# Optimization experiments

Hardware: AMD Instinct MI355X
Metric: run time of the kernel (lower is better)

## Reference

```python
import jax, jax.numpy as jnp
import numpy as np

B, C, H, W = 64, 256, 56, 56
HEADS, DH, WS = 16, 16, 7  # C = HEADS*DH
EPS = 1e-6


def setup_inputs() -> dict:
    key = jax.random.key(0)
    k1, k2, k3 = jax.random.split(key, 3)
    return {
        "x": jax.random.normal(k1, (B, C, H, W), jnp.float32),
        "bn_gamma": jnp.ones((C,), jnp.float32),
        "bn_beta": jnp.zeros((C,), jnp.float32),
        "bn_mean": jnp.zeros((C,), jnp.float32),
        "bn_var": jnp.ones((C,), jnp.float32),
        "qk_w": jax.random.normal(k2, (2 * C, C), jnp.float32) * 0.02,
        "v_w": jax.random.normal(k3, (C, C), jnp.float32) * 0.02,
    }


def reference(x, bn_gamma, bn_beta, bn_mean, bn_var, qk_w, v_w):
    Bb, Cc, Hh, Ww = x.shape
    scale = DH ** -0.5
    # eval-mode BatchNorm2d (eps=1e-6)
    inv = bn_gamma / jnp.sqrt(bn_var + EPS)
    xn = (x - bn_mean[:, None, None]) * inv[:, None, None] + bn_beta[:, None, None]
    # window partition: einops '(h1 n1)' -> h1 (window coord) OUTER, n1 INNER
    # i.e. strided/grid windows; H divisible by WS so no padding (pad_r=pad_b=0)
    n1, n2 = Hh // WS, Ww // WS
    t = xn.reshape(Bb, Cc, WS, n1, WS, n2).transpose(0, 3, 5, 2, 4, 1)  # (B,n1,n2,ws,ws,C)
    tok = t.reshape(Bb * n1 * n2, WS * WS, Cc)  # per-window tokens
    # qk: 1x1 conv == matmul; channel layout (qk, heads, dim_head)
    qk = (tok @ qk_w.T).reshape(-1, WS * WS, 2, HEADS, DH)
    q = qk[:, :, 0].transpose(0, 2, 1, 3)  # (nb, heads, hw, dh)
    k = qk[:, :, 1].transpose(0, 2, 1, 3)
    attn = jax.nn.softmax(jnp.einsum('bhqd,bhkd->bhqk', q, k) * scale, axis=-1)
    # v: 1x1 conv + ReLU (attn_pre=False path)
    v = jax.nn.relu(tok @ v_w.T).reshape(-1, WS * WS, HEADS, DH).transpose(0, 2, 1, 3)
    o = jnp.einsum('bhqk,bhkd->bhqd', attn, v)  # (nb, heads, hw, dh)
    o = o.transpose(0, 2, 1, 3).reshape(Bb, n1, n2, WS, WS, Cc)
    # inverse window merge: target (B, C, ws_h, n1, ws_w, n2) -> (B, C, H, W)
    out = o.transpose(0, 5, 3, 1, 4, 2).reshape(Bb, Cc, Hh, Ww)
    return out
```

## Files before the change

kernel.cpp:

```cpp
#include <hip/hip_runtime.h>


typedef unsigned short u16;
typedef __attribute__((ext_vector_type(4))) float f32x4;
typedef __attribute__((ext_vector_type(8))) short short8;
typedef __attribute__((ext_vector_type(4))) short short4b;

__device__ __forceinline__ u16 f2bf(float f) {
  union { float f; unsigned int i; } v; v.f = f;
  unsigned int r = v.i + 0x7fffu + ((v.i >> 16) & 1u);
  return (u16)(r >> 16);
}

__global__ __launch_bounds__(256) void k0_wpack(
    const float* __restrict__ qkw, const float* __restrict__ vw,
    u16* __restrict__ wb)
{
  int idx = blockIdx.x * 256 + threadIdx.x;
  int n = idx >> 5, oct = idx & 31;
  int head = n / 48, sub = n - head * 48;
  const float* src;
  if (sub < 16)      src = qkw + (size_t)(head * 16 + sub) * 256;
  else if (sub < 32) src = qkw + (size_t)(256 + head * 16 + (sub - 16)) * 256;
  else               src = vw  + (size_t)(head * 16 + (sub - 32)) * 256;
  src += oct * 8;
  float4 a = *(const float4*)src;
  float4 c = *(const float4*)(src + 4);
  uint4 pk;
  pk.x = (unsigned)f2bf(a.x) | ((unsigned)f2bf(a.y) << 16);
  pk.y = (unsigned)f2bf(a.z) | ((unsigned)f2bf(a.w) << 16);
  pk.z = (unsigned)f2bf(c.x) | ((unsigned)f2bf(c.y) << 16);
  pk.w = (unsigned)f2bf(c.z) | ((unsigned)f2bf(c.w) << 16);
  *(uint4*)(wb + (size_t)n * 256 + oct * 8) = pk;
}

__global__ __launch_bounds__(256) void k1_bn_gather(
    const float* __restrict__ x, const float* __restrict__ g,
    const float* __restrict__ be, const float* __restrict__ mu,
    const float* __restrict__ va, u16* __restrict__ aws)
{
  __shared__ u16 lds[56 * 264];
  const int tid = threadIdx.x;
  const int bx = blockIdx.x;
  const int ws_h = bx % 7, win_h = (bx / 7) % 8, b = bx / 56;
  const int h = ws_h * 8 + win_h;

  for (int it = 0; it < 7; ++it) {
    int idx = it * 256 + tid;
    int c = idx / 7, oct = idx % 7;
    const float* src = x + (size_t)(b * 256 + c) * 3136 + h * 56 + oct * 8;
    float4 p0 = *(const float4*)src;
    float4 p1 = *(const float4*)(src + 4);
    float inv = g[c] * rsqrtf(va[c] + 1e-6f);
    float sh = be[c] - mu[c] * inv;
    float vals[8] = { p0.x, p0.y, p0.z, p0.w, p1.x, p1.y, p1.z, p1.w };
#pragma unroll
    for (int j = 0; j < 8; ++j)
      lds[(oct * 8 + j) * 264 + c] = f2bf(fmaf(vals[j], inv, sh));
  }
  __syncthreads();

  const size_t t0 = (size_t)(b * 64 + win_h * 8) * 49;
  for (int it = 0; it < 7; ++it) {
    int idx = it * 256 + tid;
    int tl = idx >> 5, coct = idx & 31;
    int win_w = tl / 7, ws_w = tl - win_w * 7;
    int w = ws_w * 8 + win_w;
    uint4 v = *(const uint4*)&lds[w * 264 + coct * 8];
    size_t tp = t0 + (size_t)win_w * 49 + ws_h * 7 + ws_w;
    *(uint4*)(aws + tp * 256 + coct * 8) = v;
  }
}

__global__ __launch_bounds__(256, 4) void k2a_qkv(
    const u16* __restrict__ aws, const u16* __restrict__ wb,
    u16* __restrict__ qkv, int win0)
{
  __shared__ u16 sA[64 * 72];
  __shared__ u16 sB[192 * 72];
  const int tid = threadIdx.x;
  const int lane = tid & 63, wv = tid >> 6;
  const int l15 = lane & 15, quad = lane >> 4;
  const int wnb = blockIdx.x & 3;
  const int tloc = blockIdx.x >> 2;
  const size_t arow0 = (size_t)(win0 + tloc) * 49 * 256;
  const int nb0 = wnb * 192;

  f32x4 acc[4][3];
#pragma unroll
  for (int i = 0; i < 4; ++i)
#pragma unroll
    for (int j = 0; j < 3; ++j) acc[i][j] = (f32x4)(0.0f);

  for (int kb = 0; kb < 4; ++kb) {
    __syncthreads();
#pragma unroll
    for (int it = 0; it < 2; ++it) {
      int idx = it * 256 + tid;
      int r = idx >> 3, oct = idx & 7;
      int rs = r < 49 ? r : 48;
      uint4 v = *(const uint4*)(aws + arow0 + (size_t)rs * 256 + kb * 64 + oct * 8);
      *(uint4*)&sA[r * 72 + oct * 8] = v;
    }
#pragma unroll
    for (int it = 0; it < 6; ++it) {
      int idx = it * 256 + tid;
      int r = idx >> 3, oct = idx & 7;
      uint4 v = *(const uint4*)(wb + (size_t)(nb0 + r) * 256 + kb * 64 + oct * 8);
      *(uint4*)&sB[r * 72 + oct * 8] = v;
    }
    __syncthreads();
#pragma unroll
    for (int ks = 0; ks < 2; ++ks) {
      int col = ks * 32 + quad * 8;
      short8 bf[3];
#pragma unroll
      for (int nt = 0; nt < 3; ++nt)
        bf[nt] = *(const short8*)&sB[(wv * 48 + nt * 16 + l15) * 72 + col];
#pragma unroll
      for (int mt = 0; mt < 4; ++mt) {
        short8 af = *(const short8*)&sA[(mt * 16 + l15) * 72 + col];
#pragma unroll
        for (int nt = 0; nt < 3; ++nt)
          acc[mt][nt] = __builtin_amdgcn_mfma_f32_16x16x32_bf16(
              af, bf[nt], acc[mt][nt], 0, 0, 0);
      }
    }
  }

  const int head = wnb * 4 + wv;
  u16* tile = qkv + (size_t)(tloc * 16 + head) * 2400;
  u16* Qt = tile;
  u16* Kt = tile + 784;
  u16* Vt = tile + 1568;
#pragma unroll
  for (int mt = 0; mt < 4; ++mt) {
#pragma unroll
    for (int r = 0; r < 4; ++r) {
      int tok = mt * 16 + quad * 4 + r;
      if (tok < 49) {
        Qt[tok * 16 + l15] = f2bf(acc[mt][0][r]);
        Kt[tok * 16 + l15] = f2bf(acc[mt][1][r]);
      }
    }
    int tok0 = mt * 16 + quad * 4;
    if (tok0 + 3 < 49) {
      short4b pv;
#pragma unroll
      for (int r = 0; r < 4; ++r) pv[r] = (short)f2bf(fmaxf(acc[mt][2][r], 0.0f));
      *(short4b*)&Vt[l15 * 52 + tok0] = pv;
    } else if (tok0 == 48) {
      Vt[l15 * 52 + 48] = f2bf(fmaxf(acc[mt][2][0], 0.0f));
    }
  }
}

__global__ __launch_bounds__(256, 5) void k2b_attn(
    const u16* __restrict__ qkv, float* __restrict__ out, int b0)
{
  __shared__ float sO[8][16 * 52];
  const int tid = threadIdx.x;
  const int lane = tid & 63, wv = tid >> 6;
  const int l15 = lane & 15, quad = lane >> 4, kbase = quad * 4;
  const int bx = blockIdx.x;
  const int head = bx & 15;
  const int win_h = (bx >> 4) & 7;
  const int bl = bx >> 7;
  const float SM = 0.36067376022224085f;

  for (int rep = 0; rep < 2; ++rep) {
    int ww = wv * 2 + rep;
    const u16* tile = qkv +
        (size_t)(((bl * 64 + win_h * 8 + ww) * 16) + head) * 2400;
    const u16* Qt = tile;
    const u16* Kt = tile + 784;
    const u16* Vt = tile + 1568;

    short4b ka[4], qb[4];
#pragma unroll
    for (int t = 0; t < 4; ++t) {
      int rk = t * 16 + l15; rk = (rk > 48) ? 48 : rk;
      ka[t] = *(const short4b*)&Kt[rk * 16 + kbase];
      qb[t] = *(const short4b*)&Qt[rk * 16 + kbase];
    }
    f32x4 zz = (f32x4)(0.0f);
    f32x4 s[4][4];
#pragma unroll
    for (int mt = 0; mt < 4; ++mt)
#pragma unroll
      for (int nt = 0; nt < 4; ++nt)
        s[mt][nt] = __builtin_amdgcn_mfma_f32_16x16x16bf16_1k(
            ka[mt], qb[nt], zz, 0, 0, 0);

    float inv_sum[4];
    short4b pf[4][4];
#pragma unroll
    for (int nt = 0; nt < 4; ++nt) {
      float m = -1e30f;
#pragma unroll
      for (int mt = 0; mt < 4; ++mt)
#pragma unroll
        for (int r = 0; r < 4; ++r) {
          int kt = mt * 16 + kbase + r;
          float v = (kt < 49) ? s[mt][nt][r] : -1e30f;
          m = fmaxf(m, v);
        }
      m = fmaxf(m, __shfl_xor(m, 16, 64));
      m = fmaxf(m, __shfl_xor(m, 32, 64));
      float sum = 0.0f;
#pragma unroll
      for (int mt = 0; mt < 4; ++mt)
#pragma unroll
        for (int r = 0; r < 4; ++r) {
          int kt = mt * 16 + kbase + r;
          float p = (kt < 49) ? exp2f((s[mt][nt][r] - m) * SM) : 0.0f;
          sum += p;
          pf[mt][nt][r] = (short)f2bf(p);
        }
      sum += __shfl_xor(sum, 16, 64);
      sum += __shfl_xor(sum, 32, 64);
      inv_sum[nt] = 1.0f / sum;
    }

    f32x4 o[4];
#pragma unroll
    for (int nt = 0; nt < 4; ++nt) o[nt] = zz;
#pragma unroll
    for (int kt = 0; kt < 4; ++kt) {
      short4b vfrag = (short4b)0;
      if (kt < 3)
        vfrag = *(const short4b*)&Vt[l15 * 52 + kt * 16 + kbase];
      else if (quad == 0)
        vfrag[0] = (short)Vt[l15 * 52 + 48];
#pragma unroll
      for (int nt = 0; nt < 4; ++nt)
        o[nt] = __builtin_amdgcn_mfma_f32_16x16x16bf16_1k(
            vfrag, pf[kt][nt], o[nt], 0, 0, 0);
    }

    float* sOw = sO[ww];
#pragma unroll
    for (int nt = 0; nt < 4; ++nt) {
      int q = nt * 16 + l15;
      if (q < 49) {
#pragma unroll
        for (int r = 0; r < 4; ++r)
          sOw[(kbase + r) * 52 + q] = o[nt][r] * inv_sum[nt];
      }
    }
  }
  __syncthreads();

  {
    int b = b0 + bl;
    size_t obase = (size_t)(b * 256 + head * 16) * 3136;
    for (int i = tid; i < 3136; i += 256) {
      int d = i / 196, rem = i - d * 196;
      int wsh = rem / 28, dwp = rem - wsh * 28;
      int w0 = dwp * 2, w1 = w0 + 1;
      const float* sO0 = sO[w0 & 7];
      const float* sO1 = sO[w1 & 7];
      float2 val;
      val.x = sO0[d * 52 + wsh * 7 + (w0 >> 3)];
      val.y = sO1[d * 52 + wsh * 7 + (w1 >> 3)];
      *(float2*)(out + obase + (size_t)d * 3136 +
                 (wsh * 8 + win_h) * 56 + w0) = val;
    }
  }
}

extern "C" void kernel_launch(void* const* d_in, const int* in_sizes, int n_in,
                              void* d_out, int out_size, void* d_ws, size_t ws_size,
                              hipStream_t stream) {
  const float* x   = (const float*)d_in[0];
  const float* g   = (const float*)d_in[1];
  const float* be  = (const float*)d_in[2];
  const float* mu  = (const float*)d_in[3];
  const float* va  = (const float*)d_in[4];
  const float* qkw = (const float*)d_in[5];
  const float* vw  = (const float*)d_in[6];
  float* outp = (float*)d_out;

  const size_t AWS_BYTES = (size_t)200704 * 256 * 2;
  const size_t WB_BYTES  = (size_t)768 * 256 * 2;
  const size_t PER_B_QKV = (size_t)64 * 16 * 4800;

  u16* aws = (u16*)d_ws;
  u16* wb  = (u16*)((char*)d_ws + AWS_BYTES);
  u16* qkv = (u16*)((char*)d_ws + AWS_BYTES + WB_BYTES);

  size_t fixed = AWS_BYTES + WB_BYTES;
  size_t avail = ws_size > fixed ? ws_size - fixed : 0;
  int bchunk = (int)(avail / PER_B_QKV);
  if (bchunk > 64) bchunk = 64;
  if (bchunk < 1)  bchunk = 1;

  k0_wpack<<<96, 256, 0, stream>>>(qkw, vw, wb);
  k1_bn_gather<<<64 * 8 * 7, 256, 0, stream>>>(x, g, be, mu, va, aws);
  for (int c = 0; c < 64; c += bchunk) {
    int nb = (64 - c < bchunk) ? (64 - c) : bchunk;
    k2a_qkv<<<nb * 64 * 4, 256, 0, stream>>>(aws, wb, qkv, c * 64);
    k2b_attn<<<nb * 128, 256, 0, stream>>>(qkv, outp, c);
  }
}
```

Baseline: 646.3 us.

## Fuse QKV projection and window attention into one kernel via LDS

Merges the QKV GEMM kernel and the attention kernel into one kernel. Q/K/V tiles for each window and head stay in shared memory instead of round-tripping through a global qkv workspace, and the chunked launch loop goes away. Block IDs are remapped so that the 8 width-windows of a row are spread across interleaved blocks. Output is written with scattered scalar stores straight from registers instead of being staged through LDS and written as coalesced float2, which can hurt store efficiency.

```diff
diff --git a/kernel.cpp b/kernel.cpp
--- a/kernel.cpp
+++ b/kernel.cpp
@@ -72,19 +72,24 @@
   }
 }
 
-__global__ __launch_bounds__(256, 4) void k2a_qkv(
+__global__ __launch_bounds__(256, 4) void k2_fused(
     const u16* __restrict__ aws, const u16* __restrict__ wb,
-    u16* __restrict__ qkv, int win0)
+    float* __restrict__ out)
 {
-  __shared__ u16 sA[64 * 72];
-  __shared__ u16 sB[192 * 72];
+  __shared__ u16 smem[18432];
+  u16* sA = smem;
+  u16* sB = smem + 4608;
   const int tid = threadIdx.x;
   const int lane = tid & 63, wv = tid >> 6;
-  const int l15 = lane & 15, quad = lane >> 4;
-  const int wnb = blockIdx.x & 3;
-  const int tloc = blockIdx.x >> 2;
-  const size_t arow0 = (size_t)(win0 + tloc) * 49 * 256;
-  const int nb0 = wnb * 192;
+  const int l15 = lane & 15, quad = lane >> 4, kbase = quad * 4;
+
+  const int bid = blockIdx.x;
+  const int L = (bid & 7) * 2048 + (bid >> 3);
+  const int ww = L & 7, nb = (L >> 3) & 3, whg = L >> 5;
+  const int wh = whg & 7, b = whg >> 3;
+  const int tloc = (whg << 3) | ww;
+  const size_t arow0 = (size_t)tloc * 49 * 256;
+  const int nb0 = nb * 192;
 
   f32x4 acc[4][3];
 #pragma unroll
@@ -127,82 +132,64 @@
       }
     }
   }
-
-  const int head = wnb * 4 + wv;
-  u16* tile = qkv + (size_t)(tloc * 16 + head) * 2400;
-  u16* Qt = tile;
-  u16* Kt = tile + 784;
-  u16* Vt = tile + 1568;
+  __syncthreads();
+
+  u16* Qh = smem + wv * 3392;
+  u16* Kh = Qh + 1280;
+  u16* Vh = Kh + 1280;
 #pragma unroll
   for (int mt = 0; mt < 4; ++mt) {
 #pragma unroll
     for (int r = 0; r < 4; ++r) {
-      int tok = mt * 16 + quad * 4 + r;
-      if (tok < 49) {
-        Qt[tok * 16 + l15] = f2bf(acc[mt][0][r]);
-        Kt[tok * 16 + l15] = f2bf(acc[mt][1][r]);
-      }
-    }
-    int tok0 = mt * 16 + quad * 4;
-    if (tok0 + 3 < 49) {
+      int tok = mt * 16 + kbase + r;
+      Qh[tok * 20 + l15] = f2bf(acc[mt][0][r]);
+      Kh[tok * 20 + l15] = f2bf(acc[mt][1][r]);
+    }
+    int tok0 = mt * 16 + kbase;
+    if (mt < 3 || quad == 0) {
       short4b pv;
 #pragma unroll
       for (int r = 0; r < 4; ++r) pv[r] = (short)f2bf(fmaxf(acc[mt][2][r], 0.0f));
-      *(short4b*)&Vt[l15 * 52 + tok0] = pv;
-    } else if (tok0 == 48) {
-      Vt[l15 * 52 + 48] = f2bf(fmaxf(acc[mt][2][0], 0.0f));
-    }
-  }
-}
-
-__global__ __launch_bounds__(256, 5) void k2b_attn(
-    const u16* __restrict__ qkv, float* __restrict__ out, int b0)
-{
-  __shared__ float sO[8][16 * 52];
-  const int tid = threadIdx.x;
-  const int lane = tid & 63, wv = tid >> 6;
-  const int l15 = lane & 15, quad = lane >> 4, kbase = quad * 4;
-  const int bx = blockIdx.x;
-  const int head = bx & 15;
-  const int win_h = (bx >> 4) & 7;
-  const int bl = bx >> 7;
+      *(short4b*)&Vh[l15 * 52 + tok0] = pv;
+    }
+  }
+
   const float SM = 0.36067376022224085f;
-
-  for (int rep = 0; rep < 2; ++rep) {
-    int ww = wv * 2 + rep;
-    const u16* tile = qkv +
-        (size_t)(((bl * 64 + win_h * 8 + ww) * 16) + head) * 2400;
-    const u16* Qt = tile;
-    const u16* Kt = tile + 784;
-    const u16* Vt = tile + 1568;
-
-    short4b ka[4], qb[4];
-#pragma unroll
-    for (int t = 0; t < 4; ++t) {
-      int rk = t * 16 + l15; rk = (rk > 48) ? 48 : rk;
-      ka[t] = *(const short4b*)&Kt[rk * 16 + kbase];
-      qb[t] = *(const short4b*)&Qt[rk * 16 + kbase];
-    }
-    f32x4 zz = (f32x4)(0.0f);
-    f32x4 s[4][4];
+  short4b ka[4], vf[4];
+#pragma unroll
+  for (int t = 0; t < 4; ++t) {
+    ka[t] = *(const short4b*)&Kh[(t * 16 + l15) * 20 + kbase];
+    vf[t] = *(const short4b*)&Vh[l15 * 52 + t * 16 + kbase];
+  }
+  f32x4 zz = (f32x4)(0.0f);
+  const size_t obase0 = (size_t)(b * 256 + nb * 64 + wv * 16) * 3136;
+
+#pragma unroll
+  for (int qh = 0; qh < 2; ++qh) {
+    short4b qb[2];
+#pragma unroll
+    for (int ntl = 0; ntl < 2; ++ntl)
+      qb[ntl] = *(const short4b*)&Qh[((qh * 2 + ntl) * 16 + l15) * 20 + kbase];
+
+    f32x4 s[4][2];
 #pragma unroll
     for (int mt = 0; mt < 4; ++mt)
 #pragma unroll
-      for (int nt = 0; nt < 4; ++nt)
-        s[mt][nt] = __builtin_amdgcn_mfma_f32_16x16x16bf16_1k(
-            ka[mt], qb[nt], zz, 0, 0, 0);
-
-    float inv_sum[4];
-    short4b pf[4][4];
-#pragma unroll
-    for (int nt = 0; nt < 4; ++nt) {
+      for (int ntl = 0; ntl < 2; ++ntl)
+        s[mt][ntl] = __builtin_amdgcn_mfma_f32_16x16x16bf16_1k(
+            ka[mt], qb[ntl], zz, 0, 0, 0);
+
+    float inv_sum[2];
+    short4b pf[4][2];
+#pragma unroll
+    for (int ntl = 0; ntl < 2; ++ntl) {
       float m = -1e30f;
 #pragma unroll
       for (int mt = 0; mt < 4; ++mt)
 #pragma unroll
         for (int r = 0; r < 4; ++r) {
           int kt = mt * 16 + kbase + r;
-          float v = (kt < 49) ? s[mt][nt][r] : -1e30f;
+          float v = (kt < 49) ? s[mt][ntl][r] : -1e30f;
           m = fmaxf(m, v);
         }
       m = fmaxf(m, __shfl_xor(m, 16, 64));
@@ -213,58 +200,35 @@
 #pragma unroll
         for (int r = 0; r < 4; ++r) {
           int kt = mt * 16 + kbase + r;
-          float p = (kt < 49) ? exp2f((s[mt][nt][r] - m) * SM) : 0.0f;
+          float p = (kt < 49) ? exp2f((s[mt][ntl][r] - m) * SM) : 0.0f;
           sum += p;
-          pf[mt][nt][r] = (short)f2bf(p);
+          pf[mt][ntl][r] = (short)f2bf(p);
         }
       sum += __shfl_xor(sum, 16, 64);
       sum += __shfl_xor(sum, 32, 64);
-      inv_sum[nt] = 1.0f / sum;
-    }
-
-    f32x4 o[4];
-#pragma unroll
-    for (int nt = 0; nt < 4; ++nt) o[nt] = zz;
-#pragma unroll
-    for (int kt = 0; kt < 4; ++kt) {
-      short4b vfrag = (short4b)0;
-      if (kt < 3)
-        vfrag = *(const short4b*)&Vt[l15 * 52 + kt * 16 + kbase];
-      else if (quad == 0)
-        vfrag[0] = (short)Vt[l15 * 52 + 48];
-#pragma unroll
-      for (int nt = 0; nt < 4; ++nt)
-        o[nt] = __builtin_amdgcn_mfma_f32_16x16x16bf16_1k(
-            vfrag, pf[kt][nt], o[nt], 0, 0, 0);
-    }
-
-    float* sOw = sO[ww];
-#pragma unroll
-    for (int nt = 0; nt < 4; ++nt) {
-      int q = nt * 16 + l15;
+      inv_sum[ntl] = 1.0f / sum;
+    }
+
+    f32x4 o[2];
+#pragma unroll
+    for (int ntl = 0; ntl < 2; ++ntl) o[ntl] = zz;
+#pragma unroll
+    for (int kt = 0; kt < 4; ++kt)
+#pragma unroll
+      for (int ntl = 0; ntl < 2; ++ntl)
+        o[ntl] = __builtin_amdgcn_mfma_f32_16x16x16bf16_1k(
+            vf[kt], pf[kt][ntl], o[ntl], 0, 0, 0);
+
+#pragma unroll
+    for (int ntl = 0; ntl < 2; ++ntl) {
+      int q = qh * 32 + ntl * 16 + l15;
       if (q < 49) {
+        int tsh = q / 7, tsw = q - tsh * 7;
+        size_t pbase = obase0 + (size_t)(tsh * 8 + wh) * 56 + tsw * 8 + ww;
 #pragma unroll
         for (int r = 0; r < 4; ++r)
-          sOw[(kbase + r) * 52 + q] = o[nt][r] * inv_sum[nt];
+          out[pbase + (size_t)(kbase + r) * 3136] = o[ntl][r] * inv_sum[ntl];
       }
-    }
-  }
-  __syncthreads();
-
-  {
-    int b = b0 + bl;
-    size_t obase = (size_t)(b * 256 + head * 16) * 3136;
-    for (int i = tid; i < 3136; i += 256) {
-      int d = i / 196, rem = i - d * 196;
-      int wsh = rem / 28, dwp = rem - wsh * 28;
-      int w0 = dwp * 2, w1 = w0 + 1;
-      const float* sO0 = sO[w0 & 7];
-      const float* sO1 = sO[w1 & 7];
-      float2 val;
-      val.x = sO0[d * 52 + wsh * 7 + (w0 >> 3)];
-      val.y = sO1[d * 52 + wsh * 7 + (w1 >> 3)];
-      *(float2*)(out + obase + (size_t)d * 3136 +
-                 (wsh * 8 + win_h) * 56 + w0) = val;
     }
   }
 }
@@ -282,24 +246,10 @@
   float* outp = (float*)d_out;
 
   const size_t AWS_BYTES = (size_t)200704 * 256 * 2;
-  const size_t WB_BYTES  = (size_t)768 * 256 * 2;
-  const size_t PER_B_QKV = (size_t)64 * 16 * 4800;
-
   u16* aws = (u16*)d_ws;
   u16* wb  = (u16*)((char*)d_ws + AWS_BYTES);
-  u16* qkv = (u16*)((char*)d_ws + AWS_BYTES + WB_BYTES);
-
-  size_t fixed = AWS_BYTES + WB_BYTES;
-  size_t avail = ws_size > fixed ? ws_size - fixed : 0;
-  int bchunk = (int)(avail / PER_B_QKV);
-  if (bchunk > 64) bchunk = 64;
-  if (bchunk < 1)  bchunk = 1;
 
   k0_wpack<<<96, 256, 0, stream>>>(qkw, vw, wb);
   k1_bn_gather<<<64 * 8 * 7, 256, 0, stream>>>(x, g, be, mu, va, aws);
-  for (int c = 0; c < 64; c += bchunk) {
-    int nb = (64 - c < bchunk) ? (64 - c) : bchunk;
-    k2a_qkv<<<nb * 64 * 4, 256, 0, stream>>>(aws, wb, qkv, c * 64);
-    k2b_attn<<<nb * 128, 256, 0, stream>>>(qkv, outp, c);
-  }
-}
+  k2_fused<<<64 * 64 * 4, 256, 0, stream>>>(aws, wb, outp);
+}
```

After: 564.2 us. 12.7% less time.
